# Kernel optimization log

Measured on AMD Instinct MI355X. Metric: run time of the kernel, lower is better.

Reference implementation:

```python
import jax, jax.numpy as jnp
import numpy as np

N_NODES = 50000
N_EDGES = 1600000
IN_DIM, HID, HEADS, OUT_DIM = 128, 32, 4, 16
NEG_SLOPE = 0.2  # DGL GATConv default


def setup_inputs() -> dict:
    key = jax.random.key(0)
    ks = jax.random.split(key, 12)
    features = jax.random.normal(ks[0], (N_NODES, IN_DIM), dtype=jnp.float32)
    src = jax.random.randint(ks[1], (N_EDGES,), 0, N_NODES, dtype=jnp.int32)
    dst = jax.random.randint(ks[2], (N_EDGES,), 0, N_NODES, dtype=jnp.int32)
    # layer 1 params (xavier-style scale)
    W1 = jax.random.normal(ks[3], (IN_DIM, HEADS * HID), dtype=jnp.float32) * (2.0 / (IN_DIM + HEADS * HID)) ** 0.5
    al1 = jax.random.normal(ks[4], (HEADS, HID), dtype=jnp.float32) * 0.1
    ar1 = jax.random.normal(ks[5], (HEADS, HID), dtype=jnp.float32) * 0.1
    b1 = jnp.zeros((HEADS * HID,), dtype=jnp.float32)
    # layer 2 params
    W2 = jax.random.normal(ks[6], (HID, OUT_DIM), dtype=jnp.float32) * (2.0 / (HID + OUT_DIM)) ** 0.5
    al2 = jax.random.normal(ks[7], (1, OUT_DIM), dtype=jnp.float32) * 0.1
    ar2 = jax.random.normal(ks[8], (1, OUT_DIM), dtype=jnp.float32) * 0.1
    b2 = jnp.zeros((OUT_DIM,), dtype=jnp.float32)
    return {"features": features, "src": src, "dst": dst,
            "W1": W1, "al1": al1, "ar1": ar1, "b1": b1,
            "W2": W2, "al2": al2, "ar2": ar2, "b2": b2}


def gat_conv(x, src, dst, W, al, ar, b, n_nodes):
    """DGL GATConv (no dropout, no residual). Returns [N, H, out]."""
    H, out = al.shape
    feat = (x @ W).reshape(-1, H, out)                       # [N,H,out]
    el = jnp.sum(feat * al, axis=-1)                         # [N,H]
    er = jnp.sum(feat * ar, axis=-1)                         # [N,H]
    e = jax.nn.leaky_relu(el[src] + er[dst], NEG_SLOPE)      # [E,H]
    # segment softmax over incoming edges per destination node
    m = jax.ops.segment_max(e, dst, num_segments=n_nodes)    # [N,H]
    ex = jnp.exp(e - m[dst])                                 # [E,H]
    s = jax.ops.segment_sum(ex, dst, num_segments=n_nodes)   # [N,H]
    alpha = ex / s[dst]                                      # [E,H]
    msg = alpha[:, :, None] * feat[src]                      # [E,H,out]
    rst = jax.ops.segment_sum(msg, dst, num_segments=n_nodes)
    return rst + b.reshape(H, out)


def reference(features, src, dst, W1, al1, ar1, b1, W2, al2, ar2, b2):
    n = features.shape[0]
    x1 = gat_conv(features, src, dst, W1, al1, ar1, b1, n)   # [N,HEADS,HID]
    x1 = jnp.mean(jax.nn.relu(x1), axis=1)                   # [N,HID]
    x2 = gat_conv(x1, src, dst, W2, al2, ar2, b2, n)         # [N,1,OUT]
    x2 = jnp.squeeze(x2, axis=1)                             # [N,OUT]
    return jax.nn.log_softmax(x2, axis=-1)
```

## Files before the change

### kernel.cpp

```cpp
#include <hip/hip_runtime.h>
#include <hip/hip_fp16.h>
#include <math.h>

#define NEG_SLOPE 0.2f
#define BINCAP 10240

typedef __attribute__((ext_vector_type(8))) short short8;
typedef __attribute__((ext_vector_type(4))) float f32x4;

__device__ __forceinline__ float lrelu(float x) {
    return x >= 0.f ? x : NEG_SLOPE * x;
}
__device__ __forceinline__ unsigned bf16_rne(float f) {
    unsigned b = __float_as_uint(f);
    return (b + 0x7FFFu + ((b >> 16) & 1u)) >> 16;
}
__device__ __forceinline__ unsigned h2_bits(__half2 h) {
    return *(unsigned*)&h;
}
__device__ __forceinline__ __half2 bits_h2(unsigned u) {
    return *(__half2*)&u;
}
__device__ __forceinline__ unsigned short h_bits(__half h) {
    return *(unsigned short*)&h;
}

__global__ __launch_bounds__(256) void prep(
    const float* __restrict__ W1, unsigned short* __restrict__ Wt,
    int* __restrict__ bin_cursor)
{
    if (blockIdx.x == 64) {
        bin_cursor[threadIdx.x] = 0;
        return;
    }
    int i = blockIdx.x * 256 + threadIdx.x;
    int kin = i >> 7, nout = i & 127;
    Wt[nout * 128 + kin] = (unsigned short)bf16_rne(W1[kin * 128 + nout]);
}

extern "C" __global__ __launch_bounds__(256) void gemm_scatter(
    const float* __restrict__ X, const unsigned short* __restrict__ Wt,
    const float* __restrict__ al, const float* __restrict__ ar,
    const int* __restrict__ src, const int* __restrict__ dst,
    int* __restrict__ bin_cursor, unsigned* __restrict__ binned,
    unsigned short* __restrict__ feat1h, float* __restrict__ el1,
    float* __restrict__ er1, int N, int E, int nbins, int gemm_blocks)
{
    extern __shared__ char smem_raw[];
    int tid = threadIdx.x;

    if ((int)blockIdx.x >= gemm_blocks) {
        unsigned* stage = (unsigned*)smem_raw;
        int* hist   = (int*)(stage + 3328);
        int* base_l = hist + 256;
        int bid = blockIdx.x - gemm_blocks;
        hist[tid] = 0;
        __syncthreads();
        int epb = (E + 511) / 512;
        int beg = bid * epb, end = min(E, beg + epb);
        int cnt_local = end - beg;
        for (int k = tid; k < cnt_local; k += 256) {
            int d = dst[beg + k];
            stage[k] = ((unsigned)d << 16) | (unsigned)src[beg + k];
            atomicAdd(&hist[d >> 8], 1);
        }
        __syncthreads();
        if (tid < nbins) {
            int c = hist[tid];
            base_l[tid] = (c > 0) ? (tid * BINCAP + atomicAdd(&bin_cursor[tid], c)) : 0;
        }
        __syncthreads();
        hist[tid] = 0;
        __syncthreads();
        for (int k = tid; k < cnt_local; k += 256) {
            unsigned w = stage[k];
            int bin = w >> 24;
            int slot = atomicAdd(&hist[bin], 1);
            binned[base_l[bin] + slot] = w;
        }
        return;
    }

    unsigned short* Wb = (unsigned short*)smem_raw;
    int nb = blockIdx.x * 64;

    for (int idx = tid; idx < 128 * 16; idx += 256) {
        int row = idx >> 4, q = idx & 15;
        *(uint4*)&Wb[row * 138 + q * 8] = *(const uint4*)&Wt[row * 128 + q * 8];
    }
    __syncthreads();

    int wave = tid >> 6, lane = tid & 63;
    int m = lane & 15, quad = lane >> 4;
    int nx = min(nb + wave * 16 + m, N - 1);
    const float* xrow = X + (size_t)nx * 128;

    f32x4 acc[8];
#pragma unroll
    for (int t = 0; t < 8; ++t) acc[t] = (f32x4){0.f, 0.f, 0.f, 0.f};

#pragma unroll
    for (int kt = 0; kt < 4; ++kt) {
        int k0 = kt * 32 + quad * 8;
        float4 xa = *(const float4*)&xrow[k0];
        float4 xb = *(const float4*)&xrow[k0 + 4];
        uint4 pk;
        pk.x = bf16_rne(xa.x) | (bf16_rne(xa.y) << 16);
        pk.y = bf16_rne(xa.z) | (bf16_rne(xa.w) << 16);
        pk.z = bf16_rne(xb.x) | (bf16_rne(xb.y) << 16);
        pk.w = bf16_rne(xb.z) | (bf16_rne(xb.w) << 16);
        short8 a = *(short8*)&pk;
#pragma unroll
        for (int t = 0; t < 8; ++t) {
            short8 b = *(const short8*)&Wb[(t * 16 + m) * 138 + k0];
            acc[t] = __builtin_amdgcn_mfma_f32_16x16x32_bf16(a, b, acc[t], 0, 0, 0);
        }
    }

    float al_lo[4], al_hi[4], ar_lo[4], ar_hi[4];
#pragma unroll
    for (int h = 0; h < 4; ++h) {
        al_lo[h] = al[h * 32 + m];       al_hi[h] = al[h * 32 + 16 + m];
        ar_lo[h] = ar[h * 32 + m];       ar_hi[h] = ar[h * 32 + 16 + m];
    }

#pragma unroll
    for (int r = 0; r < 4; ++r) {
        int n = nb + wave * 16 + quad * 4 + r;
        float pel[4], per[4];
#pragma unroll
        for (int h = 0; h < 4; ++h) {
            float fa = acc[2 * h][r], fb = acc[2 * h + 1][r];
            pel[h] = fa * al_lo[h] + fb * al_hi[h];
            per[h] = fa * ar_lo[h] + fb * ar_hi[h];
        }
#pragma unroll
        for (int off = 1; off < 16; off <<= 1) {
#pragma unroll
            for (int h = 0; h < 4; ++h) {
                pel[h] += __shfl_xor(pel[h], off);
                per[h] += __shfl_xor(per[h], off);
            }
        }
        if (n < N) {
#pragma unroll
            for (int t = 0; t < 8; ++t)
                feat1h[(size_t)n * 128 + t * 16 + m] =
                    h_bits(__float2half_rn(acc[t][r]));
            if (m == 0) {
#pragma unroll
                for (int h = 0; h < 4; ++h) {
                    el1[(size_t)n * 4 + h] = pel[h];
                    er1[(size_t)n * 4 + h] = per[h];
                }
            }
        }
    }
}

__global__ __launch_bounds__(512) void local_sort(
    const unsigned* __restrict__ binned, const int* __restrict__ bin_cursor,
    int* __restrict__ rowptr, unsigned short* __restrict__ deg,
    unsigned short* __restrict__ csr, int N, int nbins)
{
    __shared__ int cnt[256];
    __shared__ int wsum[4];
    int b = blockIdx.x;
    int t = threadIdx.x;
    int gbase = b * BINCAP;
    int gcount = bin_cursor[b];
    if (t < 256) cnt[t] = 0;
    __syncthreads();
    for (int i = t; i < gcount; i += 512)
        atomicAdd(&cnt[(binned[gbase + i] >> 16) & 255], 1);
    __syncthreads();
    int own = (t < 256) ? cnt[t] : 0;
    int x = own;
#pragma unroll
    for (int off = 1; off < 64; off <<= 1) {
        int y = __shfl_up(x, off);
        if ((t & 63) >= off) x += y;
    }
    if (t < 256 && (t & 63) == 63) wsum[t >> 6] = x;
    __syncthreads();
    if (t < 256) {
        int wadd = 0;
        for (int wv = 0; wv < (t >> 6); ++wv) wadd += wsum[wv];
        int excl = x + wadd - own;
        int dcount = min(256, N - (b << 8));
        if (t < dcount) {
            rowptr[(b << 8) + t] = gbase + excl;
            deg[(b << 8) + t] = (unsigned short)own;
        }
        cnt[t] = excl;
    }
    __syncthreads();
    for (int i = t; i < gcount; i += 512) {
        unsigned w = binned[gbase + i];
        int slot = atomicAdd(&cnt[(w >> 16) & 255], 1);
        csr[gbase + slot] = (unsigned short)(w & 0xFFFFu);
    }
}

__global__ __launch_bounds__(256) void agg1_fused(
    const int* __restrict__ rowptr, const unsigned short* __restrict__ deg,
    const unsigned short* __restrict__ csr,
    const unsigned short* __restrict__ feat1h, const float* __restrict__ el1,
    const float* __restrict__ er1, const float* __restrict__ b1,
    const float* __restrict__ W2, const float* __restrict__ al2,
    const float* __restrict__ ar2, unsigned short* __restrict__ feat2h,
    float* __restrict__ el2, float* __restrict__ er2, int N)
{
    __shared__ uint2 pairs[4][4][66];
    int gid = blockIdx.x * 256 + threadIdx.x;
    int d = gid >> 6;
    if (d >= N) return;
    int wv = (threadIdx.x >> 6) & 3;
    int lane = threadIdx.x & 63;
    int half = lane >> 5;
    int l32 = lane & 31;
    int h32 = l32 >> 3;
    float4 er4 = ((const float4*)er1)[d];
    int beg = rowptr[d], end = beg + (int)deg[d];
    const uint2* feat64 = (const uint2*)feat1h;

    f32x4 A = {0.f, 0.f, 0.f, 0.f};
    float S = 0.f;
    const __half2 hz = __float2half2_rn(0.f);

    for (int base = beg; base < end; base += 64) {
        int cnt = min(64, end - base);
        int sn = 0;
        float4 v = make_float4(-INFINITY, -INFINITY, -INFINITY, -INFINITY);
        if (lane < cnt) {
            sn = (int)csr[base + lane];
            float4 el4 = ((const float4*)el1)[sn];
            v.x = lrelu(el4.x + er4.x);
            v.y = lrelu(el4.y + er4.y);
            v.z = lrelu(el4.z + er4.z);
            v.w = lrelu(el4.w + er4.w);
        }
        unsigned snb = (unsigned)sn << 5;
        pairs[wv][0][lane] = make_uint2(snb, h2_bits(__float2half2_rn(__expf(v.x))));
        pairs[wv][1][lane] = make_uint2(snb, h2_bits(__float2half2_rn(__expf(v.y))));
        pairs[wv][2][lane] = make_uint2(snb, h2_bits(__float2half2_rn(__expf(v.z))));
        pairs[wv][3][lane] = make_uint2(snb, h2_bits(__float2half2_rn(__expf(v.w))));

        __half2 C0 = hz, C1 = hz, D0 = hz, D1 = hz, Sh = hz;
        int cnt8 = (cnt + 7) & ~7;
        for (int i = 0; i < cnt8; i += 8) {
            uint2 p0 = pairs[wv][h32][i + half];
            uint2 p1 = pairs[wv][h32][i + 2 + half];
            uint2 p2 = pairs[wv][h32][i + 4 + half];
            uint2 p3 = pairs[wv][h32][i + 6 + half];
            uint2 u0 = feat64[p0.x + l32];
            uint2 u1 = feat64[p1.x + l32];
            uint2 u2 = feat64[p2.x + l32];
            uint2 u3 = feat64[p3.x + l32];
            __half2 w0 = bits_h2(p0.y), w1 = bits_h2(p1.y);
            __half2 w2 = bits_h2(p2.y), w3 = bits_h2(p3.y);
            C0 = __hfma2(bits_h2(u0.x), w0, C0);
            C1 = __hfma2(bits_h2(u0.y), w0, C1);
            D0 = __hfma2(bits_h2(u1.x), w1, D0);
            D1 = __hfma2(bits_h2(u1.y), w1, D1);
            C0 = __hfma2(bits_h2(u2.x), w2, C0);
            C1 = __hfma2(bits_h2(u2.y), w2, C1);
            D0 = __hfma2(bits_h2(u3.x), w3, D0);
            D1 = __hfma2(bits_h2(u3.y), w3, D1);
            Sh = __hadd2(Sh, __hadd2(w0, w1));
            Sh = __hadd2(Sh, __hadd2(w2, w3));
        }
        A.x += __low2float(C0) + __low2float(D0);
        A.y += __high2float(C0) + __high2float(D0);
        A.z += __low2float(C1) + __low2float(D1);
        A.w += __high2float(C1) + __high2float(D1);
        S += __low2float(Sh);
    }
    A.x += __shfl_xor(A.x, 32);
    A.y += __shfl_xor(A.y, 32);
    A.z += __shfl_xor(A.z, 32);
    A.w += __shfl_xor(A.w, 32);
    S   += __shfl_xor(S, 32);
    float inv = (end > beg) ? (1.f / S) : 0.f;

    float4 bb = *(const float4*)(b1 + 4 * l32);
    float r0 = fmaxf(A.x * inv + bb.x, 0.f);
    float r1 = fmaxf(A.y * inv + bb.y, 0.f);
    float r2 = fmaxf(A.z * inv + bb.z, 0.f);
    float r3 = fmaxf(A.w * inv + bb.w, 0.f);
    r0 += __shfl_xor(r0, 8); r0 += __shfl_xor(r0, 16);
    r1 += __shfl_xor(r1, 8); r1 += __shfl_xor(r1, 16);
    r2 += __shfl_xor(r2, 8); r2 += __shfl_xor(r2, 16);
    r3 += __shfl_xor(r3, 8); r3 += __shfl_xor(r3, 16);
    float u0 = 0.25f * r0, u1 = 0.25f * r1, u2 = 0.25f * r2, u3 = 0.25f * r3;

    int j = lane & 15;
    int rep = lane >> 4;
    float f2 = 0.f;
#pragma unroll
    for (int qq = 0; qq < 2; ++qq) {
        int q = 2 * rep + qq;
        float xa = __shfl(u0, q);
        float xb = __shfl(u1, q);
        float xc = __shfl(u2, q);
        float xd = __shfl(u3, q);
        const float* wrow = W2 + (4 * q) * 16 + j;
        f2 += xa * wrow[0] + xb * wrow[16] + xc * wrow[32] + xd * wrow[48];
    }
    f2 += __shfl_xor(f2, 16);
    f2 += __shfl_xor(f2, 32);

    float pel = f2 * al2[j], per = f2 * ar2[j];
#pragma unroll
    for (int off = 1; off < 16; off <<= 1) {
        pel += __shfl_xor(pel, off);
        per += __shfl_xor(per, off);
    }
    if (lane < 16) feat2h[(size_t)d * 16 + j] = h_bits(__float2half_rn(f2));
    if (lane == 0) { el2[d] = pel; er2[d] = per; }
}

__global__ __launch_bounds__(256) void agg2_fused(
    const int* __restrict__ rowptr, const unsigned short* __restrict__ deg,
    const unsigned short* __restrict__ csr,
    const unsigned short* __restrict__ feat2h, const float* __restrict__ el2,
    const float* __restrict__ er2, const float* __restrict__ b2,
    float* __restrict__ out, int N)
{
    __shared__ uint2 pairs2[4][64];
    int gid = blockIdx.x * 256 + threadIdx.x;
    int d = gid >> 6;
    if (d >= N) return;
    int wv = (threadIdx.x >> 6) & 3;
    int lane = threadIdx.x & 63;
    int sub = lane >> 3, pr = lane & 7;
    float er = er2[d];
    int beg = rowptr[d], end = beg + (int)deg[d];
    const unsigned* feat32 = (const unsigned*)feat2h;
    const __half2 hz = __float2half2_rn(0.f);

    float S = 0.f, a0 = 0.f, a1 = 0.f;
    for (int cb = beg; cb < end; cb += 64) {
        int cnt = min(64, end - cb);
        int sn = 0;
        float v = -INFINITY;
        if (lane < cnt) {
            sn = (int)csr[cb + lane];
            v = lrelu(el2[sn] + er);
        }
        float w = __expf(v);
        pairs2[wv][lane] = make_uint2((unsigned)sn << 3,
                                      h2_bits(__float2half2_rn(w)));

        __half2 Ah = hz, Bh = hz, Sh = hz;
        int cnt16 = (cnt + 15) & ~15;
        for (int i = sub; i < cnt16; i += 16) {
            uint2 p0 = pairs2[wv][i];
            uint2 p1 = pairs2[wv][i + 8];
            unsigned u0 = feat32[p0.x + pr];
            unsigned u1 = feat32[p1.x + pr];
            __half2 w0 = bits_h2(p0.y), w1 = bits_h2(p1.y);
            Ah = __hfma2(bits_h2(u0), w0, Ah);
            Bh = __hfma2(bits_h2(u1), w1, Bh);
            Sh = __hadd2(Sh, __hadd2(w0, w1));
        }
        a0 += __low2float(Ah) + __low2float(Bh);
        a1 += __high2float(Ah) + __high2float(Bh);
        S += __low2float(Sh);
    }
    a0 += __shfl_xor(a0, 8);  a1 += __shfl_xor(a1, 8);  S += __shfl_xor(S, 8);
    a0 += __shfl_xor(a0, 16); a1 += __shfl_xor(a1, 16); S += __shfl_xor(S, 16);
    a0 += __shfl_xor(a0, 32); a1 += __shfl_xor(a1, 32); S += __shfl_xor(S, 32);
    float inv = (end > beg) ? (1.f / S) : 0.f;
    float2 bb = *(const float2*)(b2 + 2 * pr);
    float v0 = a0 * inv + bb.x;
    float v1 = a1 * inv + bb.y;
    float mm = fmaxf(v0, v1);
#pragma unroll
    for (int off = 1; off < 8; off <<= 1)
        mm = fmaxf(mm, __shfl_xor(mm, off));
    float ssum = __expf(v0 - mm) + __expf(v1 - mm);
#pragma unroll
    for (int off = 1; off < 8; off <<= 1)
        ssum += __shfl_xor(ssum, off);
    float lse = mm + __logf(ssum);
    if (lane < 8)
        *(float2*)(out + (size_t)d * 16 + 2 * pr) = make_float2(v0 - lse, v1 - lse);
}

extern "C" void kernel_launch(void* const* d_in, const int* in_sizes, int n_in,
                              void* d_out, int out_size, void* d_ws, size_t ws_size,
                              hipStream_t stream)
{
    const float* X   = (const float*)d_in[0];
    const int*   src = (const int*)d_in[1];
    const int*   dst = (const int*)d_in[2];
    const float* W1  = (const float*)d_in[3];
    const float* al1 = (const float*)d_in[4];
    const float* ar1 = (const float*)d_in[5];
    const float* b1  = (const float*)d_in[6];
    const float* W2  = (const float*)d_in[7];
    const float* al2 = (const float*)d_in[8];
    const float* ar2 = (const float*)d_in[9];
    const float* b2  = (const float*)d_in[10];
    int N = in_sizes[0] / 128;
    int E = in_sizes[1];
    int nbins = (N + 255) >> 8;

    float* ws = (float*)d_ws;
    size_t o = 0;
    unsigned short* feat1h = (unsigned short*)(ws + o); o += (size_t)N * 64;
    float* el1   = ws + o; o += (size_t)N * 4;
    float* er1   = ws + o; o += (size_t)N * 4;
    unsigned short* feat2h = (unsigned short*)(ws + o); o += (size_t)N * 8;
    float* el2   = ws + o; o += (size_t)N;
    float* er2   = ws + o; o += (size_t)N;
    int* rowptr  = (int*)(ws + o); o += (size_t)N;
    unsigned short* deg = (unsigned short*)(ws + o); o += (size_t)N / 2 + 1;
    unsigned short* Wt1b = (unsigned short*)(ws + o); o += 128 * 128 / 2;
    int* bin_cursor = (int*)(ws + o); o += 256;
    unsigned* binned = (unsigned*)(ws + o); o += (size_t)nbins * BINCAP;
    unsigned short* csr = (unsigned short*)(ws + o); o += (size_t)nbins * BINCAP / 2 + 1;
    float* out = (float*)d_out;

    prep<<<65, 256, 0, stream>>>(W1, Wt1b, bin_cursor);

    int gemm_blocks = (N + 63) / 64;
    gemm_scatter<<<gemm_blocks + 512, 256, 128 * 138 * 2, stream>>>(
        X, Wt1b, al1, ar1, src, dst, bin_cursor, binned,
        feat1h, el1, er1, N, E, nbins, gemm_blocks);

    local_sort<<<nbins, 512, 0, stream>>>(binned, bin_cursor, rowptr, deg, csr, N, nbins);

    agg1_fused<<<(N * 64 + 255) / 256, 256, 0, stream>>>(
        rowptr, deg, csr, feat1h, el1, er1, b1, W2, al2, ar2, feat2h, el2, er2, N);

    agg2_fused<<<(N * 64 + 255) / 256, 256, 0, stream>>>(
        rowptr, deg, csr, feat2h, el2, er2, b2, out, N);
}
```

Measured before the change: 218.7 us.

## Process two destination nodes per wavefront in layer-1 aggregation

```diff
diff --git a/kernel.cpp b/kernel.cpp
--- a/kernel.cpp
+++ b/kernel.cpp
@@ -211,113 +211,183 @@
     const float* __restrict__ ar2, unsigned short* __restrict__ feat2h,
     float* __restrict__ el2, float* __restrict__ er2, int N)
 {
-    __shared__ uint2 pairs[4][4][66];
+    __shared__ uint2 pairs[4][2][4][66];
     int gid = blockIdx.x * 256 + threadIdx.x;
-    int d = gid >> 6;
-    if (d >= N) return;
+    int wid = gid >> 6;
+    int d0 = 2 * wid;
+    if (d0 >= N) return;
+    int d1 = d0 + 1;
+    bool has1 = d1 < N;
     int wv = (threadIdx.x >> 6) & 3;
     int lane = threadIdx.x & 63;
     int half = lane >> 5;
     int l32 = lane & 31;
     int h32 = l32 >> 3;
-    float4 er4 = ((const float4*)er1)[d];
-    int beg = rowptr[d], end = beg + (int)deg[d];
+    float4 er4_0 = ((const float4*)er1)[d0];
+    float4 er4_1 = has1 ? ((const float4*)er1)[d1] : er4_0;
+    int beg0 = rowptr[d0], n0 = (int)deg[d0];
+    int beg1 = has1 ? rowptr[d1] : 0;
+    int n1 = has1 ? (int)deg[d1] : 0;
     const uint2* feat64 = (const uint2*)feat1h;
-
-    f32x4 A = {0.f, 0.f, 0.f, 0.f};
-    float S = 0.f;
     const __half2 hz = __float2half2_rn(0.f);
 
-    for (int base = beg; base < end; base += 64) {
-        int cnt = min(64, end - base);
-        int sn = 0;
-        float4 v = make_float4(-INFINITY, -INFINITY, -INFINITY, -INFINITY);
-        if (lane < cnt) {
-            sn = (int)csr[base + lane];
-            float4 el4 = ((const float4*)el1)[sn];
-            v.x = lrelu(el4.x + er4.x);
-            v.y = lrelu(el4.y + er4.y);
-            v.z = lrelu(el4.z + er4.z);
-            v.w = lrelu(el4.w + er4.w);
-        }
-        unsigned snb = (unsigned)sn << 5;
-        pairs[wv][0][lane] = make_uint2(snb, h2_bits(__float2half2_rn(__expf(v.x))));
-        pairs[wv][1][lane] = make_uint2(snb, h2_bits(__float2half2_rn(__expf(v.y))));
-        pairs[wv][2][lane] = make_uint2(snb, h2_bits(__float2half2_rn(__expf(v.z))));
-        pairs[wv][3][lane] = make_uint2(snb, h2_bits(__float2half2_rn(__expf(v.w))));
-
-        __half2 C0 = hz, C1 = hz, D0 = hz, D1 = hz, Sh = hz;
-        int cnt8 = (cnt + 7) & ~7;
-        for (int i = 0; i < cnt8; i += 8) {
-            uint2 p0 = pairs[wv][h32][i + half];
-            uint2 p1 = pairs[wv][h32][i + 2 + half];
-            uint2 p2 = pairs[wv][h32][i + 4 + half];
-            uint2 p3 = pairs[wv][h32][i + 6 + half];
-            uint2 u0 = feat64[p0.x + l32];
-            uint2 u1 = feat64[p1.x + l32];
-            uint2 u2 = feat64[p2.x + l32];
-            uint2 u3 = feat64[p3.x + l32];
-            __half2 w0 = bits_h2(p0.y), w1 = bits_h2(p1.y);
-            __half2 w2 = bits_h2(p2.y), w3 = bits_h2(p3.y);
-            C0 = __hfma2(bits_h2(u0.x), w0, C0);
-            C1 = __hfma2(bits_h2(u0.y), w0, C1);
-            D0 = __hfma2(bits_h2(u1.x), w1, D0);
-            D1 = __hfma2(bits_h2(u1.y), w1, D1);
-            C0 = __hfma2(bits_h2(u2.x), w2, C0);
-            C1 = __hfma2(bits_h2(u2.y), w2, C1);
-            D0 = __hfma2(bits_h2(u3.x), w3, D0);
-            D1 = __hfma2(bits_h2(u3.y), w3, D1);
-            Sh = __hadd2(Sh, __hadd2(w0, w1));
-            Sh = __hadd2(Sh, __hadd2(w2, w3));
-        }
-        A.x += __low2float(C0) + __low2float(D0);
-        A.y += __high2float(C0) + __high2float(D0);
-        A.z += __low2float(C1) + __low2float(D1);
-        A.w += __high2float(C1) + __high2float(D1);
-        S += __low2float(Sh);
-    }
-    A.x += __shfl_xor(A.x, 32);
-    A.y += __shfl_xor(A.y, 32);
-    A.z += __shfl_xor(A.z, 32);
-    A.w += __shfl_xor(A.w, 32);
-    S   += __shfl_xor(S, 32);
-    float inv = (end > beg) ? (1.f / S) : 0.f;
-
-    float4 bb = *(const float4*)(b1 + 4 * l32);
-    float r0 = fmaxf(A.x * inv + bb.x, 0.f);
-    float r1 = fmaxf(A.y * inv + bb.y, 0.f);
-    float r2 = fmaxf(A.z * inv + bb.z, 0.f);
-    float r3 = fmaxf(A.w * inv + bb.w, 0.f);
-    r0 += __shfl_xor(r0, 8); r0 += __shfl_xor(r0, 16);
-    r1 += __shfl_xor(r1, 8); r1 += __shfl_xor(r1, 16);
-    r2 += __shfl_xor(r2, 8); r2 += __shfl_xor(r2, 16);
-    r3 += __shfl_xor(r3, 8); r3 += __shfl_xor(r3, 16);
-    float u0 = 0.25f * r0, u1 = 0.25f * r1, u2 = 0.25f * r2, u3 = 0.25f * r3;
-
+    f32x4 A0 = {0.f, 0.f, 0.f, 0.f}, A1 = {0.f, 0.f, 0.f, 0.f};
+    float S0f = 0.f, S1f = 0.f;
+
+    int nmax = max(n0, n1);
+    for (int c = 0; c < nmax; c += 64) {
+        int cnt0 = min(64, n0 - c); if (cnt0 < 0) cnt0 = 0;
+        int cnt1 = min(64, n1 - c); if (cnt1 < 0) cnt1 = 0;
+
+        if (cnt0 > 0) {
+            int sn = 0;
+            float4 v = make_float4(-INFINITY, -INFINITY, -INFINITY, -INFINITY);
+            if (lane < cnt0) {
+                sn = (int)csr[beg0 + c + lane];
+                float4 el4 = ((const float4*)el1)[sn];
+                v.x = lrelu(el4.x + er4_0.x);
+                v.y = lrelu(el4.y + er4_0.y);
+                v.z = lrelu(el4.z + er4_0.z);
+                v.w = lrelu(el4.w + er4_0.w);
+            }
+            unsigned snb = (unsigned)sn << 5;
+            pairs[wv][0][0][lane] = make_uint2(snb, h2_bits(__float2half2_rn(__expf(v.x))));
+            pairs[wv][0][1][lane] = make_uint2(snb, h2_bits(__float2half2_rn(__expf(v.y))));
+            pairs[wv][0][2][lane] = make_uint2(snb, h2_bits(__float2half2_rn(__expf(v.z))));
+            pairs[wv][0][3][lane] = make_uint2(snb, h2_bits(__float2half2_rn(__expf(v.w))));
+        }
+        if (cnt1 > 0) {
+            int sn = 0;
+            float4 v = make_float4(-INFINITY, -INFINITY, -INFINITY, -INFINITY);
+            if (lane < cnt1) {
+                sn = (int)csr[beg1 + c + lane];
+                float4 el4 = ((const float4*)el1)[sn];
+                v.x = lrelu(el4.x + er4_1.x);
+                v.y = lrelu(el4.y + er4_1.y);
+                v.z = lrelu(el4.z + er4_1.z);
+                v.w = lrelu(el4.w + er4_1.w);
+            }
+            unsigned snb = (unsigned)sn << 5;
+            pairs[wv][1][0][lane] = make_uint2(snb, h2_bits(__float2half2_rn(__expf(v.x))));
+            pairs[wv][1][1][lane] = make_uint2(snb, h2_bits(__float2half2_rn(__expf(v.y))));
+            pairs[wv][1][2][lane] = make_uint2(snb, h2_bits(__float2half2_rn(__expf(v.z))));
+            pairs[wv][1][3][lane] = make_uint2(snb, h2_bits(__float2half2_rn(__expf(v.w))));
+        }
+
+        if (cnt0 > 0) {
+            __half2 C0 = hz, C1 = hz, D0 = hz, D1 = hz, Sh = hz;
+            int cnt8 = (cnt0 + 7) & ~7;
+            for (int i = 0; i < cnt8; i += 8) {
+                uint2 p0 = pairs[wv][0][h32][i + half];
+                uint2 p1 = pairs[wv][0][h32][i + 2 + half];
+                uint2 p2 = pairs[wv][0][h32][i + 4 + half];
+                uint2 p3 = pairs[wv][0][h32][i + 6 + half];
+                uint2 u0 = feat64[p0.x + l32];
+                uint2 u1 = feat64[p1.x + l32];
+                uint2 u2 = feat64[p2.x + l32];
+                uint2 u3 = feat64[p3.x + l32];
+                __half2 w0 = bits_h2(p0.y), w1 = bits_h2(p1.y);
+                __half2 w2 = bits_h2(p2.y), w3 = bits_h2(p3.y);
+                C0 = __hfma2(bits_h2(u0.x), w0, C0);
+                C1 = __hfma2(bits_h2(u0.y), w0, C1);
+                D0 = __hfma2(bits_h2(u1.x), w1, D0);
+                D1 = __hfma2(bits_h2(u1.y), w1, D1);
+                C0 = __hfma2(bits_h2(u2.x), w2, C0);
+                C1 = __hfma2(bits_h2(u2.y), w2, C1);
+                D0 = __hfma2(bits_h2(u3.x), w3, D0);
+                D1 = __hfma2(bits_h2(u3.y), w3, D1);
+                Sh = __hadd2(Sh, __hadd2(w0, w1));
+                Sh = __hadd2(Sh, __hadd2(w2, w3));
+            }
+            A0.x += __low2float(C0) + __low2float(D0);
+            A0.y += __high2float(C0) + __high2float(D0);
+            A0.z += __low2float(C1) + __low2float(D1);
+            A0.w += __high2float(C1) + __high2float(D1);
+            S0f += __low2float(Sh);
+        }
+        if (cnt1 > 0) {
+            __half2 C0 = hz, C1 = hz, D0 = hz, D1 = hz, Sh = hz;
+            int cnt8 = (cnt1 + 7) & ~7;
+            for (int i = 0; i < cnt8; i += 8) {
+                uint2 p0 = pairs[wv][1][h32][i + half];
+                uint2 p1 = pairs[wv][1][h32][i + 2 + half];
+                uint2 p2 = pairs[wv][1][h32][i + 4 + half];
+                uint2 p3 = pairs[wv][1][h32][i + 6 + half];
+                uint2 u0 = feat64[p0.x + l32];
+                uint2 u1 = feat64[p1.x + l32];
+                uint2 u2 = feat64[p2.x + l32];
+                uint2 u3 = feat64[p3.x + l32];
+                __half2 w0 = bits_h2(p0.y), w1 = bits_h2(p1.y);
+                __half2 w2 = bits_h2(p2.y), w3 = bits_h2(p3.y);
+                C0 = __hfma2(bits_h2(u0.x), w0, C0);
+                C1 = __hfma2(bits_h2(u0.y), w0, C1);
+                D0 = __hfma2(bits_h2(u1.x), w1, D0);
+                D1 = __hfma2(bits_h2(u1.y), w1, D1);
+                C0 = __hfma2(bits_h2(u2.x), w2, C0);
+                C1 = __hfma2(bits_h2(u2.y), w2, C1);
+                D0 = __hfma2(bits_h2(u3.x), w3, D0);
+                D1 = __hfma2(bits_h2(u3.y), w3, D1);
+                Sh = __hadd2(Sh, __hadd2(w0, w1));
+                Sh = __hadd2(Sh, __hadd2(w2, w3));
+            }
+            A1.x += __low2float(C0) + __low2float(D0);
+            A1.y += __high2float(C0) + __high2float(D0);
+            A1.z += __low2float(C1) + __low2float(D1);
+            A1.w += __high2float(C1) + __high2float(D1);
+            S1f += __low2float(Sh);
+        }
+    }
+
+    float4 bb4 = *(const float4*)(b1 + 4 * l32);
     int j = lane & 15;
     int rep = lane >> 4;
-    float f2 = 0.f;
-#pragma unroll
-    for (int qq = 0; qq < 2; ++qq) {
-        int q = 2 * rep + qq;
-        float xa = __shfl(u0, q);
-        float xb = __shfl(u1, q);
-        float xc = __shfl(u2, q);
-        float xd = __shfl(u3, q);
-        const float* wrow = W2 + (4 * q) * 16 + j;
-        f2 += xa * wrow[0] + xb * wrow[16] + xc * wrow[32] + xd * wrow[48];
-    }
-    f2 += __shfl_xor(f2, 16);
-    f2 += __shfl_xor(f2, 32);
-
-    float pel = f2 * al2[j], per = f2 * ar2[j];
-#pragma unroll
-    for (int off = 1; off < 16; off <<= 1) {
-        pel += __shfl_xor(pel, off);
-        per += __shfl_xor(per, off);
-    }
-    if (lane < 16) feat2h[(size_t)d * 16 + j] = h_bits(__float2half_rn(f2));
-    if (lane == 0) { el2[d] = pel; er2[d] = per; }
+#pragma unroll
+    for (int dd = 0; dd < 2; ++dd) {
+        if (dd == 1 && !has1) break;
+        f32x4 A = dd ? A1 : A0;
+        float S = dd ? S1f : S0f;
+        int d = dd ? d1 : d0;
+        int nd = dd ? n1 : n0;
+        A.x += __shfl_xor(A.x, 32);
+        A.y += __shfl_xor(A.y, 32);
+        A.z += __shfl_xor(A.z, 32);
+        A.w += __shfl_xor(A.w, 32);
+        S   += __shfl_xor(S, 32);
+        float inv = (nd > 0) ? (1.f / S) : 0.f;
+
+        float r0 = fmaxf(A.x * inv + bb4.x, 0.f);
+        float r1 = fmaxf(A.y * inv + bb4.y, 0.f);
+        float r2 = fmaxf(A.z * inv + bb4.z, 0.f);
+        float r3 = fmaxf(A.w * inv + bb4.w, 0.f);
+        r0 += __shfl_xor(r0, 8); r0 += __shfl_xor(r0, 16);
+        r1 += __shfl_xor(r1, 8); r1 += __shfl_xor(r1, 16);
+        r2 += __shfl_xor(r2, 8); r2 += __shfl_xor(r2, 16);
+        r3 += __shfl_xor(r3, 8); r3 += __shfl_xor(r3, 16);
+        float u0 = 0.25f * r0, u1 = 0.25f * r1, u2 = 0.25f * r2, u3 = 0.25f * r3;
+
+        float f2 = 0.f;
+#pragma unroll
+        for (int qq = 0; qq < 2; ++qq) {
+            int q = 2 * rep + qq;
+            float xa = __shfl(u0, q);
+            float xb = __shfl(u1, q);
+            float xc = __shfl(u2, q);
+            float xd = __shfl(u3, q);
+            const float* wrow = W2 + (4 * q) * 16 + j;
+            f2 += xa * wrow[0] + xb * wrow[16] + xc * wrow[32] + xd * wrow[48];
+        }
+        f2 += __shfl_xor(f2, 16);
+        f2 += __shfl_xor(f2, 32);
+
+        float pel = f2 * al2[j], per = f2 * ar2[j];
+#pragma unroll
+        for (int off = 1; off < 16; off <<= 1) {
+            pel += __shfl_xor(pel, off);
+            per += __shfl_xor(per, off);
+        }
+        if (lane < 16) feat2h[(size_t)d * 16 + j] = h_bits(__float2half_rn(f2));
+        if (lane == 0) { el2[d] = pel; er2[d] = per; }
+    }
 }
 
 __global__ __launch_bounds__(256) void agg2_fused(
@@ -432,7 +502,8 @@
 
     local_sort<<<nbins, 512, 0, stream>>>(binned, bin_cursor, rowptr, deg, csr, N, nbins);
 
-    agg1_fused<<<(N * 64 + 255) / 256, 256, 0, stream>>>(
+    int npairs = (N + 1) / 2;
+    agg1_fused<<<(npairs * 64 + 255) / 256, 256, 0, stream>>>(
         rowptr, deg, csr, feat1h, el1, er1, b1, W2, al2, ar2, feat2h, el2, er2, N);
 
     agg2_fused<<<(N * 64 + 255) / 256, 256, 0, stream>>>(
```

Result: no change. 220.5 us (+0.8%).
